# Kernel tuning notes

Measured on AMD Instinct MI355X. Metric: run time of the kernel, lower is better.

Reference implementation:

```python
import jax, jax.numpy as jnp
import numpy as np

B, C, H, W = 4, 256, 128, 128
RATION = 1
Cr = C // RATION


def conv1x1(x, Wt, b):
    # pointwise conv: [B,C,H,W] x [O,C] -> [B,O,H,W]
    return jnp.einsum('bchw,oc->bohw', x, Wt) + b[None, :, None, None]


def setup_inputs() -> dict:
    key = jax.random.key(0)
    ks = jax.random.split(key, 10)
    s_in = 1.0 / np.sqrt(C)
    s_up = 1.0 / np.sqrt(Cr)
    return {
        'x': jax.random.normal(ks[0], (B, C, H, W), dtype=jnp.float32),
        'Wq': jax.random.normal(ks[1], (Cr, C), dtype=jnp.float32) * s_in,
        'bq': jax.random.normal(ks[2], (Cr,), dtype=jnp.float32) * s_in,
        'Wk': jax.random.normal(ks[3], (Cr, C), dtype=jnp.float32) * s_in,
        'bk': jax.random.normal(ks[4], (Cr,), dtype=jnp.float32) * s_in,
        'Wv': jax.random.normal(ks[5], (Cr, C), dtype=jnp.float32) * s_in,
        'bv': jax.random.normal(ks[6], (Cr,), dtype=jnp.float32) * s_in,
        'Wu': jax.random.normal(ks[7], (C, Cr), dtype=jnp.float32) * s_up,
        'bu': jax.random.normal(ks[8], (C,), dtype=jnp.float32) * s_up,
        'gamma': jax.random.normal(ks[9], (1,), dtype=jnp.float32) * 0.1,
    }


def reference(x, Wq, bq, Wk, bk, Wv, bv, Wu, bu, gamma):
    b, c, h, w = x.shape
    # Q/K/V: relu(1x1 conv), then raw contiguous reshape [B,Cr,H,W] -> [B,W,Cr*H]
    x_Qw = jax.nn.relu(conv1x1(x, Wq, bq)).reshape(b, w, -1)              # [B, W, Cr*H]
    x_Kw = jnp.swapaxes(jax.nn.relu(conv1x1(x, Wk, bk)).reshape(b, w, -1), 1, 2)  # [B, Cr*H, W]
    x_Vw = jnp.swapaxes(jax.nn.relu(conv1x1(x, Wv, bv)).reshape(b, w, -1), 1, 2)  # [B, Cr*H, W]
    # attention over Width axis; softmax over dim=1 as in the original
    attn = jax.nn.softmax(jnp.matmul(x_Qw, x_Kw), axis=1)                 # [B, W, W]
    out1 = jnp.matmul(x_Vw, attn)                                         # [B, Cr*H, W]
    out = out1.reshape(b, c // RATION, h, w) * gamma
    out_w = conv1x1(out, Wu, bu)                                          # [B, C, H, W]
    return (out_w, x_Qw, x_Kw, x_Vw, gamma, attn)
```

## Files before the change

### kernel.cpp

```cpp
#include <hip/hip_runtime.h>
#include <hip/hip_bf16.h>


typedef __attribute__((ext_vector_type(8))) short bf16x8;
typedef __attribute__((ext_vector_type(4))) float f4;

#define MFMA16(a, b, c) __builtin_amdgcn_mfma_f32_16x16x32_bf16(a, b, c, 0, 0, 0)

__device__ __forceinline__ unsigned short f2bf(float f) {
  union { float f; unsigned u; } v; v.f = f;
  unsigned r = v.u + 0x7fffu + ((v.u >> 16) & 1u);
  return (unsigned short)(r >> 16);
}
__device__ __forceinline__ float bf2f(unsigned short h) {
  union { unsigned u; float f; } v; v.u = ((unsigned)h) << 16;
  return v.f;
}
__device__ __forceinline__ void splitf(float f, unsigned short &hi, unsigned short &lo) {
  unsigned short h = f2bf(f);
  hi = h; lo = f2bf(f - bf2f(h));
}

__device__ __forceinline__ void split8t(float4 a, float4 b, bf16x8 &hi, bf16x8 &lo) {
  union { bf16x8 v; unsigned u[4]; } uh, ul;
  const unsigned* ua = (const unsigned*)&a;
  const unsigned* ub = (const unsigned*)&b;
  const float* fa = (const float*)&a;
  const float* fb = (const float*)&b;
#pragma unroll
  for (int e = 0; e < 2; ++e) {
    uh.u[e]     = __builtin_amdgcn_perm(ua[2*e+1], ua[2*e], 0x07060302u);
    uh.u[2 + e] = __builtin_amdgcn_perm(ub[2*e+1], ub[2*e], 0x07060302u);
    union { float f; unsigned u; } p0, p1, q0, q1;
    p0.u = ua[2*e] & 0xffff0000u;   p1.u = ua[2*e+1] & 0xffff0000u;
    p0.f = fa[2*e] - p0.f;          p1.f = fa[2*e+1] - p1.f;
    ul.u[e] = __builtin_amdgcn_perm(p1.u, p0.u, 0x07060302u);
    q0.u = ub[2*e] & 0xffff0000u;   q1.u = ub[2*e+1] & 0xffff0000u;
    q0.f = fb[2*e] - q0.f;          q1.f = fb[2*e+1] - q1.f;
    ul.u[2 + e] = __builtin_amdgcn_perm(q1.u, q0.u, 0x07060302u);
  }
  hi = uh.v; lo = ul.v;
}

__device__ __forceinline__ bf16x8 pack8t(float4 a, float4 b) {
  union { bf16x8 v; unsigned u[4]; } r;
  const unsigned* ua = (const unsigned*)&a;
  const unsigned* ub = (const unsigned*)&b;
  r.u[0] = __builtin_amdgcn_perm(ua[1], ua[0], 0x07060302u);
  r.u[1] = __builtin_amdgcn_perm(ua[3], ua[2], 0x07060302u);
  r.u[2] = __builtin_amdgcn_perm(ub[1], ub[0], 0x07060302u);
  r.u[3] = __builtin_amdgcn_perm(ub[3], ub[2], 0x07060302u);
  return r.v;
}

__global__ __launch_bounds__(256) void k_prep(
    const float* __restrict__ Wq, const float* __restrict__ Wk,
    const float* __restrict__ Wv, const float* __restrict__ Wu,
    unsigned short* __restrict__ wqh, unsigned short* __restrict__ wql,
    unsigned short* __restrict__ wkh, unsigned short* __restrict__ wkl,
    unsigned short* __restrict__ wvh, unsigned short* __restrict__ wuh) {
  const int i = blockIdx.x * 256 + threadIdx.x;
  unsigned short h, lo2;
  splitf(Wq[i], h, lo2); wqh[i] = h; wql[i] = lo2;
  splitf(Wk[i], h, lo2); wkh[i] = h; wkl[i] = lo2;
  wvh[i] = f2bf(Wv[i]);
  wuh[i] = f2bf(Wu[i]);
}

__global__ __launch_bounds__(256, 4) void k_qkv(
    const float* __restrict__ x,
    const unsigned short* __restrict__ wqh, const unsigned short* __restrict__ wql,
    const unsigned short* __restrict__ wkh, const unsigned short* __restrict__ wkl,
    const unsigned short* __restrict__ wvh,
    const float* __restrict__ bq, const float* __restrict__ bk,
    const float* __restrict__ bv,
    float* __restrict__ outQ, float* __restrict__ outKT, float* __restrict__ outVT,
    float* __restrict__ K2f) {
  const int pb = blockIdx.x, b = blockIdx.y;
  const int p0 = pb * 32;
  const int t = threadIdx.x;

  __shared__ __align__(16) unsigned short xthi[32][264];
  __shared__ __align__(16) unsigned short xtlo[32][264];
  float (*tbuf)[132] = reinterpret_cast<float (*)[132]>(&xtlo[0][0]);

  {
    const int cp = t & 127;
    const int hh = (t >> 7) * 16;
    const float* r0 = x + ((size_t)b * 256 + 2 * cp) * 16384 + p0 + hh;
    const float* r1 = r0 + 16384;
#pragma unroll
    for (int q = 0; q < 4; ++q) {
      float4 v0 = *(const float4*)(r0 + 4 * q);
      float4 v1 = *(const float4*)(r1 + 4 * q);
      const unsigned* u0 = (const unsigned*)&v0;
      const unsigned* u1 = (const unsigned*)&v1;
      const float* f0 = (const float*)&v0;
      const float* f1 = (const float*)&v1;
#pragma unroll
      for (int e = 0; e < 4; ++e) {
        const int p = hh + 4 * q + e;
        *(unsigned*)&xthi[p][2 * cp] = __builtin_amdgcn_perm(u1[e], u0[e], 0x07060302u);
        union { float f; unsigned u; } l0, l1;
        l0.u = u0[e] & 0xffff0000u;  l1.u = u1[e] & 0xffff0000u;
        l0.f = f0[e] - l0.f;         l1.f = f1[e] - l1.f;
        *(unsigned*)&xtlo[p][2 * cp] = __builtin_amdgcn_perm(l1.u, l0.u, 0x07060302u);
      }
    }
  }
  __syncthreads();

  const int wv = t >> 6, l = t & 63;
  const int lr = l & 15, lkq = l >> 4, lk = lkq * 8;
  const size_t ob = (size_t)b * 4194304;
  const f4 fz = {0.f, 0.f, 0.f, 0.f};
  f4 acc[4][2];

#define CONV_PASS(WHI, WLO, SPLIT)                                        \
  {                                                                       \
    _Pragma("unroll") for (int mt = 0; mt < 4; ++mt)                      \
    _Pragma("unroll") for (int nt = 0; nt < 2; ++nt) acc[mt][nt] = fz;    \
    _Pragma("unroll 1") for (int kk = 0; kk < 8; ++kk) {                  \
      const int c0 = kk * 32 + lk;                                        \
      bf16x8 ahi[4], alo[4], bhi[2], blo[2];                              \
      _Pragma("unroll") for (int mt = 0; mt < 4; ++mt) {                  \
        const int o = wv * 64 + mt * 16 + lr;                             \
        ahi[mt] = *(const bf16x8*)(WHI + o * 256 + c0);                   \
        if (SPLIT) alo[mt] = *(const bf16x8*)(WLO + o * 256 + c0);        \
      }                                                                   \
      _Pragma("unroll") for (int nt = 0; nt < 2; ++nt) {                  \
        bhi[nt] = *(const bf16x8*)&xthi[nt * 16 + lr][c0];                \
        if (SPLIT) blo[nt] = *(const bf16x8*)&xtlo[nt * 16 + lr][c0];     \
      }                                                                   \
      _Pragma("unroll") for (int mt = 0; mt < 4; ++mt)                    \
      _Pragma("unroll") for (int nt = 0; nt < 2; ++nt) {                  \
        acc[mt][nt] = MFMA16(ahi[mt], bhi[nt], acc[mt][nt]);              \
        if (SPLIT) {                                                      \
          acc[mt][nt] = MFMA16(ahi[mt], blo[nt], acc[mt][nt]);            \
          acc[mt][nt] = MFMA16(alo[mt], bhi[nt], acc[mt][nt]);            \
        }                                                                 \
      }                                                                   \
    }                                                                     \
  }

#define TRANSPOSE_OUT(DST)                                                   \
  _Pragma("unroll") for (int par = 0; par < 2; ++par) {                      \
    __syncthreads();                                                         \
    _Pragma("unroll") for (int mt = 0; mt < 4; ++mt)                         \
    _Pragma("unroll") for (int m = 0; m < 2; ++m) {                          \
      const int i = wv * 32 + mt * 8 + lkq * 2 + m;                          \
      const int e = par + 2 * m;       \
      _Pragma("unroll") for (int nt = 0; nt < 2; ++nt)                       \
        tbuf[nt * 16 + lr][i] = acc[mt][nt][e];                              \
    }                                                                        \
    __syncthreads();                                                         \
    {                                                                        \
      const int pr = t >> 3, c4 = (t & 7) * 16;                              \
      float* dst = DST + ob + (size_t)(par * 16384 + p0 + pr) * 128 + c4;    \
      _Pragma("unroll") for (int q2 = 0; q2 < 4; ++q2)                       \
        *(float4*)(dst + 4 * q2) = *(const float4*)&tbuf[pr][c4 + 4 * q2];   \
    }                                                                        \
  }

  CONV_PASS(wqh, wql, 1)
  {
    const int rbase = wv * 64 + lkq * 4;
#pragma unroll
    for (int mt = 0; mt < 4; ++mt)
#pragma unroll
      for (int e = 0; e < 4; ++e) {
        const int o = rbase + mt * 16 + e;
        const float bb = bq[o];
#pragma unroll
        for (int nt = 0; nt < 2; ++nt)
          outQ[ob + (size_t)o * 16384 + (p0 + nt * 16 + lr)] =
              fmaxf(acc[mt][nt][e] + bb, 0.0f);
      }
  }

  CONV_PASS(wkh, wkl, 1)
  {
    const int rbase = wv * 64 + lkq * 4;
#pragma unroll
    for (int mt = 0; mt < 4; ++mt)
#pragma unroll
      for (int e = 0; e < 4; ++e) {
        const int o = rbase + mt * 16 + e;
        const float bb = bk[o];
#pragma unroll
        for (int nt = 0; nt < 2; ++nt) {
          const float v = fmaxf(acc[mt][nt][e] + bb, 0.0f);
          acc[mt][nt][e] = v;
          K2f[ob + (size_t)o * 16384 + (p0 + nt * 16 + lr)] = v;
        }
      }
  }
  TRANSPOSE_OUT(outKT)

  CONV_PASS(wvh, wvh, 0)
  {
    const int rbase = wv * 64 + lkq * 4;
#pragma unroll
    for (int mt = 0; mt < 4; ++mt)
#pragma unroll
      for (int e = 0; e < 4; ++e) {
        const int o = rbase + mt * 16 + e;
        const float bb = bv[o];
#pragma unroll
        for (int nt = 0; nt < 2; ++nt)
          acc[mt][nt][e] = fmaxf(acc[mt][nt][e] + bb, 0.0f);
      }
  }
  TRANSPOSE_OUT(outVT)
#undef CONV_PASS
#undef TRANSPOSE_OUT
}

__global__ __launch_bounds__(512, 4) void k_qk(
    const float* __restrict__ Q2, const float* __restrict__ K2f,
    float* __restrict__ Spart) {
  const int s = blockIdx.x, b = blockIdx.y;
  const int t = threadIdx.x;
  const int wvv = t >> 6, l = t & 63;
  const int wm = (wvv >> 2) * 64, wn = (wvv & 3) * 32;
  const int lr = l & 15, lkq = l >> 4, lk = lkq * 8;
  const size_t qb = (size_t)b * 4194304;
  const int jb = s * 256;
  const f4 fz = {0.f, 0.f, 0.f, 0.f};
  f4 acc[4][2];
#pragma unroll
  for (int mt = 0; mt < 4; ++mt)
#pragma unroll
    for (int nt = 0; nt < 2; ++nt) acc[mt][nt] = fz;

#pragma unroll 1
  for (int kk = 0; kk < 8; ++kk) {
    const int j = jb + kk * 32 + lk;
    bf16x8 ahi[4], alo[4], bhi[2], blo[2];
#pragma unroll
    for (int mt = 0; mt < 4; ++mt) {
      const float* r = Q2 + qb + (size_t)(wm + mt * 16 + lr) * 32768 + j;
      split8t(*(const float4*)r, *(const float4*)(r + 4), ahi[mt], alo[mt]);
    }
#pragma unroll
    for (int nt = 0; nt < 2; ++nt) {
      const float* r = K2f + qb + (size_t)(wn + nt * 16 + lr) * 32768 + j;
      split8t(*(const float4*)r, *(const float4*)(r + 4), bhi[nt], blo[nt]);
    }
#pragma unroll
    for (int mt = 0; mt < 4; ++mt)
#pragma unroll
      for (int nt = 0; nt < 2; ++nt) {
        acc[mt][nt] = MFMA16(ahi[mt], bhi[nt], acc[mt][nt]);
        acc[mt][nt] = MFMA16(ahi[mt], blo[nt], acc[mt][nt]);
        acc[mt][nt] = MFMA16(alo[mt], bhi[nt], acc[mt][nt]);
      }
  }
  float* out = Spart + ((size_t)(b * 128 + s)) * 16384;
#pragma unroll
  for (int mt = 0; mt < 4; ++mt)
#pragma unroll
    for (int e = 0; e < 4; ++e) {
      const int i1 = wm + mt * 16 + lkq * 4 + e;
#pragma unroll
      for (int nt = 0; nt < 2; ++nt)
        out[i1 * 128 + (wn + nt * 16 + lr)] = acc[mt][nt][e];
    }
}

__global__ __launch_bounds__(256) void k_sred(
    const float* __restrict__ Spart, float* __restrict__ S) {
  const int e = blockIdx.x * 256 + threadIdx.x;
  const int b = blockIdx.y;
  const float* p = Spart + (size_t)b * 128 * 16384 + e;
  float s0 = 0.f, s1 = 0.f, s2 = 0.f, s3 = 0.f;
#pragma unroll 4
  for (int s = 0; s < 128; s += 4) {
    s0 += p[(size_t)s * 16384];
    s1 += p[(size_t)(s + 1) * 16384];
    s2 += p[(size_t)(s + 2) * 16384];
    s3 += p[(size_t)(s + 3) * 16384];
  }
  S[b * 16384 + e] = (s0 + s1) + (s2 + s3);
}

__global__ __launch_bounds__(256) void k_softmax(
    const float* __restrict__ S, const float* __restrict__ gin,
    float* __restrict__ attnO, float* __restrict__ gammaO,
    unsigned short* __restrict__ attnTg) {
  const int cb = blockIdx.x, b = blockIdx.y;
  const int t = threadIdx.x;
  const int col = cb * 8 + (t >> 5);
  const int r = t & 31;
  const float* Sb = S + b * 16384;
  float v[4];
#pragma unroll
  for (int j = 0; j < 4; ++j) v[j] = Sb[(r + 32 * j) * 128 + col];
  float m = fmaxf(fmaxf(v[0], v[1]), fmaxf(v[2], v[3]));
#pragma unroll
  for (int k = 16; k >= 1; k >>= 1) m = fmaxf(m, __shfl_xor(m, k, 32));
  float sum = 0.f;
#pragma unroll
  for (int j = 0; j < 4; ++j) { v[j] = expf(v[j] - m); sum += v[j]; }
#pragma unroll
  for (int k = 16; k >= 1; k >>= 1) sum += __shfl_xor(sum, k, 32);
  const float inv = 1.0f / sum;
  const float g = gin[0];
#pragma unroll
  for (int j = 0; j < 4; ++j) {
    const float p2 = v[j] * inv;
    attnO[b * 16384 + (r + 32 * j) * 128 + col] = p2;
    attnTg[(size_t)b * 16384 + (size_t)col * 128 + (r + 32 * j)] = f2bf(p2 * g);
  }
  if (b == 0 && cb == 0 && t == 0) gammaO[0] = gin[0];
}

__global__ __launch_bounds__(256) void k_pv(
    const float* __restrict__ VT, const unsigned short* __restrict__ attnTg,
    unsigned short* __restrict__ outb) {
  const int jblk = blockIdx.x, b = blockIdx.y;
  const int t = threadIdx.x;
  const int wvv = t >> 6, l = t & 63;
  const int lr = l & 15, lkq = l >> 4, lk = lkq * 8;
  const size_t vb = (size_t)b * 4194304;
  const int j0 = jblk * 256 + wvv * 64;
  const f4 fz = {0.f, 0.f, 0.f, 0.f};
  f4 acc[4][8];
#pragma unroll
  for (int mt = 0; mt < 4; ++mt)
#pragma unroll
    for (int nt = 0; nt < 8; ++nt) acc[mt][nt] = fz;

#pragma unroll
  for (int kk = 0; kk < 4; ++kk) {
    const int k0 = kk * 32 + lk;
    bf16x8 av[4], bt[8];
#pragma unroll
    for (int mt = 0; mt < 4; ++mt) {
      const float* r = VT + vb + (size_t)(j0 + mt * 16 + lr) * 128 + k0;
      av[mt] = pack8t(*(const float4*)r, *(const float4*)(r + 4));
    }
#pragma unroll
    for (int nt = 0; nt < 8; ++nt)
      bt[nt] = *(const bf16x8*)(attnTg + (size_t)b * 16384 +
                                (size_t)(nt * 16 + lr) * 128 + k0);
#pragma unroll
    for (int mt = 0; mt < 4; ++mt)
#pragma unroll
      for (int nt = 0; nt < 8; ++nt)
        acc[mt][nt] = MFMA16(av[mt], bt[nt], acc[mt][nt]);
  }
#pragma unroll
  for (int mt = 0; mt < 4; ++mt)
#pragma unroll
    for (int e = 0; e < 4; ++e) {
      const int j = j0 + mt * 16 + lkq * 4 + e;
#pragma unroll
      for (int nt = 0; nt < 8; ++nt)
        outb[vb + (size_t)j * 128 + (nt * 16 + lr)] = f2bf(acc[mt][nt][e]);
    }
}

__global__ __launch_bounds__(256) void k_up(
    const unsigned short* __restrict__ outb, const unsigned short* __restrict__ wuh,
    const float* __restrict__ bu, float* __restrict__ outw) {
  const int pb = blockIdx.x, b = blockIdx.y;
  const int p0 = pb * 64;
  const int t = threadIdx.x;
  __shared__ unsigned short ot[64][264];
  {
    const int cp = t & 127;
    const int ph = (t >> 7) * 32;
    const unsigned short* row0 = outb + ((size_t)b * 256 + 2 * cp) * 16384 + p0 + ph;
    const unsigned* r0 = (const unsigned*)row0;
    const unsigned* r1 = (const unsigned*)(row0 + 16384);
#pragma unroll
    for (int k = 0; k < 16; ++k) {
      const unsigned a0 = r0[k], a1 = r1[k];
      const int p = ph + 2 * k;
      *(unsigned*)&ot[p][2 * cp] = (a0 & 0xffffu) | (a1 << 16);
      *(unsigned*)&ot[p + 1][2 * cp] = (a0 >> 16) | (a1 & 0xffff0000u);
    }
  }
  __syncthreads();
  const int wv = t >> 6, l = t & 63;
  const int lr = l & 15, lkq = l >> 4, lk = lkq * 8;
  const f4 fz = {0.f, 0.f, 0.f, 0.f};
  f4 acc[4][4];
#pragma unroll
  for (int mt = 0; mt < 4; ++mt)
#pragma unroll
    for (int nt = 0; nt < 4; ++nt) acc[mt][nt] = fz;

#pragma unroll 1
  for (int kk = 0; kk < 8; ++kk) {
    const int c0 = kk * 32 + lk;
    bf16x8 a[4], bt[4];
#pragma unroll
    for (int mt = 0; mt < 4; ++mt)
      a[mt] = *(const bf16x8*)(wuh + (wv * 64 + mt * 16 + lr) * 256 + c0);
#pragma unroll
    for (int nt = 0; nt < 4; ++nt)
      bt[nt] = *(const bf16x8*)&ot[nt * 16 + lr][c0];
#pragma unroll
    for (int mt = 0; mt < 4; ++mt)
#pragma unroll
      for (int nt = 0; nt < 4; ++nt)
        acc[mt][nt] = MFMA16(a[mt], bt[nt], acc[mt][nt]);
  }
  const size_t ob2 = (size_t)b * 4194304;
  const int rbase = wv * 64 + lkq * 4;
#pragma unroll
  for (int mt = 0; mt < 4; ++mt)
#pragma unroll
    for (int e = 0; e < 4; ++e) {
      const int o = rbase + mt * 16 + e;
      const float bb = bu[o];
#pragma unroll
      for (int nt = 0; nt < 4; ++nt)
        outw[ob2 + (size_t)o * 16384 + (p0 + nt * 16 + lr)] = acc[mt][nt][e] + bb;
    }
}

extern "C" void kernel_launch(void* const* d_in, const int* in_sizes, int n_in,
                              void* d_out, int out_size, void* d_ws, size_t ws_size,
                              hipStream_t stream) {
  (void)in_sizes; (void)n_in; (void)out_size; (void)ws_size;
  const float* x  = (const float*)d_in[0];
  const float* Wq = (const float*)d_in[1];
  const float* bq = (const float*)d_in[2];
  const float* Wk = (const float*)d_in[3];
  const float* bk = (const float*)d_in[4];
  const float* Wv = (const float*)d_in[5];
  const float* bv = (const float*)d_in[6];
  const float* Wu = (const float*)d_in[7];
  const float* bu = (const float*)d_in[8];
  const float* gm = (const float*)d_in[9];

  float* dout   = (float*)d_out;
  float* outw   = dout;
  float* outQ   = dout + 16777216;
  float* outKT  = dout + 33554432;
  float* outVT  = dout + 50331648;
  float* gammaO = dout + 67108864;
  float* attnO  = dout + 67108865;

  char* wsb = (char*)d_ws;
  float* K2f   = (float*)(wsb);
  float* Spart = (float*)(wsb + 67108864);
  unsigned short* outb = (unsigned short*)(wsb + 67108864);
  float* S     = (float*)(wsb + 100663296);
  unsigned short* attnTg = (unsigned short*)(wsb + 100925440);
  unsigned short* wqh = (unsigned short*)(wsb + 101056512);
  unsigned short* wql = wqh + 65536;
  unsigned short* wkh = wql + 65536;
  unsigned short* wkl = wkh + 65536;
  unsigned short* wvh = wkl + 65536;
  unsigned short* wuh = wvh + 65536;

  k_prep<<<dim3(256), dim3(256), 0, stream>>>(Wq, Wk, Wv, Wu,
                                              wqh, wql, wkh, wkl, wvh, wuh);
  k_qkv<<<dim3(512, 4), dim3(256), 0, stream>>>(x, wqh, wql, wkh, wkl, wvh,
                                                bq, bk, bv,
                                                outQ, outKT, outVT, K2f);
  k_qk<<<dim3(128, 4), dim3(512), 0, stream>>>(outQ, K2f, Spart);
  k_sred<<<dim3(64, 4), dim3(256), 0, stream>>>(Spart, S);
  k_softmax<<<dim3(16, 4), dim3(256), 0, stream>>>(S, gm, attnO, gammaO, attnTg);
  k_pv<<<dim3(128, 4), dim3(256), 0, stream>>>(outVT, attnTg, outb);
  k_up<<<dim3(256, 4), dim3(256), 0, stream>>>(outb, wuh, bu, outw);
}
```

Measured before the change: 591.5 us.

## Drop K2f scratch copy; read K from transposed output via LDS in QK

```diff
diff --git a/kernel.cpp b/kernel.cpp
--- a/kernel.cpp
+++ b/kernel.cpp
@@ -74,47 +74,50 @@
     const unsigned short* __restrict__ wvh,
     const float* __restrict__ bq, const float* __restrict__ bk,
     const float* __restrict__ bv,
-    float* __restrict__ outQ, float* __restrict__ outKT, float* __restrict__ outVT,
-    float* __restrict__ K2f) {
-  const int pb = blockIdx.x, b = blockIdx.y;
-  const int p0 = pb * 32;
+    float* __restrict__ outQ, float* __restrict__ outKT, float* __restrict__ outVT) {
+  const int pbv = blockIdx.x, b = blockIdx.y;
   const int t = threadIdx.x;
 
   __shared__ __align__(16) unsigned short xthi[32][264];
   __shared__ __align__(16) unsigned short xtlo[32][264];
   float (*tbuf)[132] = reinterpret_cast<float (*)[132]>(&xtlo[0][0]);
-
-  {
-    const int cp = t & 127;
-    const int hh = (t >> 7) * 16;
-    const float* r0 = x + ((size_t)b * 256 + 2 * cp) * 16384 + p0 + hh;
-    const float* r1 = r0 + 16384;
-#pragma unroll
-    for (int q = 0; q < 4; ++q) {
-      float4 v0 = *(const float4*)(r0 + 4 * q);
-      float4 v1 = *(const float4*)(r1 + 4 * q);
-      const unsigned* u0 = (const unsigned*)&v0;
-      const unsigned* u1 = (const unsigned*)&v1;
-      const float* f0 = (const float*)&v0;
-      const float* f1 = (const float*)&v1;
-#pragma unroll
-      for (int e = 0; e < 4; ++e) {
-        const int p = hh + 4 * q + e;
-        *(unsigned*)&xthi[p][2 * cp] = __builtin_amdgcn_perm(u1[e], u0[e], 0x07060302u);
-        union { float f; unsigned u; } l0, l1;
-        l0.u = u0[e] & 0xffff0000u;  l1.u = u1[e] & 0xffff0000u;
-        l0.f = f0[e] - l0.f;         l1.f = f1[e] - l1.f;
-        *(unsigned*)&xtlo[p][2 * cp] = __builtin_amdgcn_perm(l1.u, l0.u, 0x07060302u);
-      }
-    }
-  }
-  __syncthreads();
 
   const int wv = t >> 6, l = t & 63;
   const int lr = l & 15, lkq = l >> 4, lk = lkq * 8;
   const size_t ob = (size_t)b * 4194304;
   const f4 fz = {0.f, 0.f, 0.f, 0.f};
   f4 acc[4][2];
+
+#pragma unroll 1
+  for (int st = 0; st < 2; ++st) {
+    const int p0 = pbv * 64 + st * 32;
+    __syncthreads();
+
+    {
+      const int cp = t & 127;
+      const int hh = (t >> 7) * 16;
+      const float* r0 = x + ((size_t)b * 256 + 2 * cp) * 16384 + p0 + hh;
+      const float* r1 = r0 + 16384;
+#pragma unroll
+      for (int q = 0; q < 4; ++q) {
+        float4 v0 = *(const float4*)(r0 + 4 * q);
+        float4 v1 = *(const float4*)(r1 + 4 * q);
+        const unsigned* u0 = (const unsigned*)&v0;
+        const unsigned* u1 = (const unsigned*)&v1;
+        const float* f0 = (const float*)&v0;
+        const float* f1 = (const float*)&v1;
+#pragma unroll
+        for (int e = 0; e < 4; ++e) {
+          const int p = hh + 4 * q + e;
+          *(unsigned*)&xthi[p][2 * cp] = __builtin_amdgcn_perm(u1[e], u0[e], 0x07060302u);
+          union { float f; unsigned u; } l0, l1;
+          l0.u = u0[e] & 0xffff0000u;  l1.u = u1[e] & 0xffff0000u;
+          l0.f = f0[e] - l0.f;         l1.f = f1[e] - l1.f;
+          *(unsigned*)&xtlo[p][2 * cp] = __builtin_amdgcn_perm(l1.u, l0.u, 0x07060302u);
+        }
+      }
+    }
+    __syncthreads();
 
 #define CONV_PASS(WHI, WLO, SPLIT)                                        \
   {                                                                       \
@@ -149,7 +152,7 @@
     _Pragma("unroll") for (int mt = 0; mt < 4; ++mt)                         \
     _Pragma("unroll") for (int m = 0; m < 2; ++m) {                          \
       const int i = wv * 32 + mt * 8 + lkq * 2 + m;                          \
-      const int e = par + 2 * m;       \
+      const int e = par + 2 * m;                                             \
       _Pragma("unroll") for (int nt = 0; nt < 2; ++nt)                       \
         tbuf[nt * 16 + lr][i] = acc[mt][nt][e];                              \
     }                                                                        \
@@ -162,62 +165,60 @@
     }                                                                        \
   }
 
-  CONV_PASS(wqh, wql, 1)
-  {
-    const int rbase = wv * 64 + lkq * 4;
-#pragma unroll
-    for (int mt = 0; mt < 4; ++mt)
-#pragma unroll
-      for (int e = 0; e < 4; ++e) {
-        const int o = rbase + mt * 16 + e;
-        const float bb = bq[o];
-#pragma unroll
-        for (int nt = 0; nt < 2; ++nt)
-          outQ[ob + (size_t)o * 16384 + (p0 + nt * 16 + lr)] =
-              fmaxf(acc[mt][nt][e] + bb, 0.0f);
-      }
-  }
-
-  CONV_PASS(wkh, wkl, 1)
-  {
-    const int rbase = wv * 64 + lkq * 4;
-#pragma unroll
-    for (int mt = 0; mt < 4; ++mt)
-#pragma unroll
-      for (int e = 0; e < 4; ++e) {
-        const int o = rbase + mt * 16 + e;
-        const float bb = bk[o];
-#pragma unroll
-        for (int nt = 0; nt < 2; ++nt) {
-          const float v = fmaxf(acc[mt][nt][e] + bb, 0.0f);
-          acc[mt][nt][e] = v;
-          K2f[ob + (size_t)o * 16384 + (p0 + nt * 16 + lr)] = v;
+    CONV_PASS(wqh, wql, 1)
+    {
+      const int rbase = wv * 64 + lkq * 4;
+#pragma unroll
+      for (int mt = 0; mt < 4; ++mt)
+#pragma unroll
+        for (int e = 0; e < 4; ++e) {
+          const int o = rbase + mt * 16 + e;
+          const float bb = bq[o];
+#pragma unroll
+          for (int nt = 0; nt < 2; ++nt)
+            outQ[ob + (size_t)o * 16384 + (p0 + nt * 16 + lr)] =
+                fmaxf(acc[mt][nt][e] + bb, 0.0f);
         }
-      }
-  }
-  TRANSPOSE_OUT(outKT)
-
-  CONV_PASS(wvh, wvh, 0)
-  {
-    const int rbase = wv * 64 + lkq * 4;
-#pragma unroll
-    for (int mt = 0; mt < 4; ++mt)
-#pragma unroll
-      for (int e = 0; e < 4; ++e) {
-        const int o = rbase + mt * 16 + e;
-        const float bb = bv[o];
-#pragma unroll
-        for (int nt = 0; nt < 2; ++nt)
-          acc[mt][nt][e] = fmaxf(acc[mt][nt][e] + bb, 0.0f);
-      }
-  }
-  TRANSPOSE_OUT(outVT)
+    }
+
+    CONV_PASS(wkh, wkl, 1)
+    {
+      const int rbase = wv * 64 + lkq * 4;
+#pragma unroll
+      for (int mt = 0; mt < 4; ++mt)
+#pragma unroll
+        for (int e = 0; e < 4; ++e) {
+          const int o = rbase + mt * 16 + e;
+          const float bb = bk[o];
+#pragma unroll
+          for (int nt = 0; nt < 2; ++nt)
+            acc[mt][nt][e] = fmaxf(acc[mt][nt][e] + bb, 0.0f);
+        }
+    }
+    TRANSPOSE_OUT(outKT)
+
+    CONV_PASS(wvh, wvh, 0)
+    {
+      const int rbase = wv * 64 + lkq * 4;
+#pragma unroll
+      for (int mt = 0; mt < 4; ++mt)
+#pragma unroll
+        for (int e = 0; e < 4; ++e) {
+          const int o = rbase + mt * 16 + e;
+          const float bb = bv[o];
+#pragma unroll
+          for (int nt = 0; nt < 2; ++nt)
+            acc[mt][nt][e] = fmaxf(acc[mt][nt][e] + bb, 0.0f);
+        }
+    }
+    TRANSPOSE_OUT(outVT)
 #undef CONV_PASS
 #undef TRANSPOSE_OUT
-}
-
-__global__ __launch_bounds__(512, 4) void k_qk(
-    const float* __restrict__ Q2, const float* __restrict__ K2f,
+  }
+}
+
+__global__ __launch_bounds__(512, 2) void k_qk(
+    const float* __restrict__ Q2, const float* __restrict__ KT,
     float* __restrict__ Spart) {
   const int s = blockIdx.x, b = blockIdx.y;
   const int t = threadIdx.x;
@@ -226,6 +227,10 @@
   const int lr = l & 15, lkq = l >> 4, lk = lkq * 8;
   const size_t qb = (size_t)b * 4194304;
   const int jb = s * 256;
+
+  __shared__ __align__(16) unsigned short khi[128][136];
+  __shared__ __align__(16) unsigned short klo[128][136];
+
   const f4 fz = {0.f, 0.f, 0.f, 0.f};
   f4 acc[4][2];
 #pragma unroll
@@ -234,28 +239,51 @@
     for (int nt = 0; nt < 2; ++nt) acc[mt][nt] = fz;
 
 #pragma unroll 1
-  for (int kk = 0; kk < 8; ++kk) {
-    const int j = jb + kk * 32 + lk;
-    bf16x8 ahi[4], alo[4], bhi[2], blo[2];
-#pragma unroll
-    for (int mt = 0; mt < 4; ++mt) {
-      const float* r = Q2 + qb + (size_t)(wm + mt * 16 + lr) * 32768 + j;
-      split8t(*(const float4*)r, *(const float4*)(r + 4), ahi[mt], alo[mt]);
-    }
-#pragma unroll
-    for (int nt = 0; nt < 2; ++nt) {
-      const float* r = K2f + qb + (size_t)(wn + nt * 16 + lr) * 32768 + j;
-      split8t(*(const float4*)r, *(const float4*)(r + 4), bhi[nt], blo[nt]);
-    }
-#pragma unroll
-    for (int mt = 0; mt < 4; ++mt)
+  for (int jt = 0; jt < 2; ++jt) {
+    const int jsub = jb + jt * 128;
+    __syncthreads();
+#pragma unroll
+    for (int it = 0; it < 8; ++it) {
+      const int idx = it * 512 + t;
+      const int jg = idx >> 5, i2c = (idx & 31) * 4;
+      float4 v = *(const float4*)(KT + qb + (size_t)(jsub + jg) * 128 + i2c);
+      const float* fv = (const float*)&v;
+#pragma unroll
+      for (int e = 0; e < 4; ++e) {
+        union { float f; unsigned u; } w; w.f = fv[e];
+        const unsigned short hi = (unsigned short)(w.u >> 16);
+        union { unsigned u; float f; } hf; hf.u = (unsigned)hi << 16;
+        khi[i2c + e][jg] = hi;
+        klo[i2c + e][jg] = f2bf(w.f - hf.f);
+      }
+    }
+    __syncthreads();
+
+#pragma unroll 1
+    for (int kk = 0; kk < 4; ++kk) {
+      const int jloc = kk * 32 + lk;
+      bf16x8 ahi[4], alo[4], bhi[2], blo[2];
+#pragma unroll
+      for (int mt = 0; mt < 4; ++mt) {
+        const float* r = Q2 + qb + (size_t)(wm + mt * 16 + lr) * 32768 + jsub + jloc;
+        split8t(*(const float4*)r, *(const float4*)(r + 4), ahi[mt], alo[mt]);
+      }
 #pragma unroll
       for (int nt = 0; nt < 2; ++nt) {
-        acc[mt][nt] = MFMA16(ahi[mt], bhi[nt], acc[mt][nt]);
-        acc[mt][nt] = MFMA16(ahi[mt], blo[nt], acc[mt][nt]);
-        acc[mt][nt] = MFMA16(alo[mt], bhi[nt], acc[mt][nt]);
+        bhi[nt] = *(const bf16x8*)&khi[wn + nt * 16 + lr][jloc];
+        blo[nt] = *(const bf16x8*)&klo[wn + nt * 16 + lr][jloc];
       }
-  }
+#pragma unroll
+      for (int mt = 0; mt < 4; ++mt)
+#pragma unroll
+        for (int nt = 0; nt < 2; ++nt) {
+          acc[mt][nt] = MFMA16(ahi[mt], bhi[nt], acc[mt][nt]);
+          acc[mt][nt] = MFMA16(ahi[mt], blo[nt], acc[mt][nt]);
+          acc[mt][nt] = MFMA16(alo[mt], bhi[nt], acc[mt][nt]);
+        }
+    }
+  }
+
   float* out = Spart + ((size_t)(b * 128 + s)) * 16384;
 #pragma unroll
   for (int mt = 0; mt < 4; ++mt)
@@ -364,62 +392,70 @@
 __global__ __launch_bounds__(256) void k_up(
     const unsigned short* __restrict__ outb, const unsigned short* __restrict__ wuh,
     const float* __restrict__ bu, float* __restrict__ outw) {
-  const int pb = blockIdx.x, b = blockIdx.y;
-  const int p0 = pb * 64;
+  const int pbv = blockIdx.x, b = blockIdx.y;
   const int t = threadIdx.x;
   __shared__ unsigned short ot[64][264];
-  {
-    const int cp = t & 127;
-    const int ph = (t >> 7) * 32;
-    const unsigned short* row0 = outb + ((size_t)b * 256 + 2 * cp) * 16384 + p0 + ph;
-    const unsigned* r0 = (const unsigned*)row0;
-    const unsigned* r1 = (const unsigned*)(row0 + 16384);
-#pragma unroll
-    for (int k = 0; k < 16; ++k) {
-      const unsigned a0 = r0[k], a1 = r1[k];
-      const int p = ph + 2 * k;
-      *(unsigned*)&ot[p][2 * cp] = (a0 & 0xffffu) | (a1 << 16);
-      *(unsigned*)&ot[p + 1][2 * cp] = (a0 >> 16) | (a1 & 0xffff0000u);
-    }
-  }
-  __syncthreads();
   const int wv = t >> 6, l = t & 63;
   const int lr = l & 15, lkq = l >> 4, lk = lkq * 8;
   const f4 fz = {0.f, 0.f, 0.f, 0.f};
-  f4 acc[4][4];
-#pragma unroll
-  for (int mt = 0; mt < 4; ++mt)
-#pragma unroll
-    for (int nt = 0; nt < 4; ++nt) acc[mt][nt] = fz;
+  const size_t ob2 = (size_t)b * 4194304;
 
 #pragma unroll 1
-  for (int kk = 0; kk < 8; ++kk) {
-    const int c0 = kk * 32 + lk;
-    bf16x8 a[4], bt[4];
+  for (int st = 0; st < 2; ++st) {
+    const int p0 = pbv * 128 + st * 64;
+    __syncthreads();
+    {
+      const int cp = t & 127;
+      const int ph = (t >> 7) * 32;
+      const unsigned short* row0 = outb + ((size_t)b * 256 + 2 * cp) * 16384 + p0 + ph;
+      const unsigned* r0 = (const unsigned*)row0;
+      const unsigned* r1 = (const unsigned*)(row0 + 16384);
+#pragma unroll
+      for (int k = 0; k < 16; ++k) {
+        const unsigned a0 = r0[k], a1 = r1[k];
+        const int p = ph + 2 * k;
+        *(unsigned*)&ot[p][2 * cp] = (a0 & 0xffffu) | (a1 << 16);
+        *(unsigned*)&ot[p + 1][2 * cp] = (a0 >> 16) | (a1 & 0xffff0000u);
+      }
+    }
+    __syncthreads();
+
+    f4 acc[4][4];
 #pragma unroll
     for (int mt = 0; mt < 4; ++mt)
-      a[mt] = *(const bf16x8*)(wuh + (wv * 64 + mt * 16 + lr) * 256 + c0);
-#pragma unroll
-    for (int nt = 0; nt < 4; ++nt)
-      bt[nt] = *(const bf16x8*)&ot[nt * 16 + lr][c0];
+#pragma unroll
+      for (int nt = 0; nt < 4; ++nt) acc[mt][nt] = fz;
+
+#pragma unroll 1
+    for (int kk = 0; kk < 8; ++kk) {
+      const int c0 = kk * 32 + lk;
+      bf16x8 a[4], bt[4];
+#pragma unroll
+      for (int mt = 0; mt < 4; ++mt)
+        a[mt] = *(const bf16x8*)(wuh + (wv * 64 + mt * 16 + lr) * 256 + c0);
+#pragma unroll
+      for (int nt = 0; nt < 4; ++nt)
+        bt[nt] = *(const bf16x8*)&ot[nt * 16 + lr][c0];
+#pragma unroll
+      for (int mt = 0; mt < 4; ++mt)
+#pragma unroll
+        for (int nt = 0; nt < 4; ++nt)
+          acc[mt][nt] = MFMA16(a[mt], bt[nt], acc[mt][nt]);
+    }
+    const int rbase = wv * 64 + lkq * 4;
 #pragma unroll
     for (int mt = 0; mt < 4; ++mt)
 #pragma unroll
-      for (int nt = 0; nt < 4; ++nt)
-        acc[mt][nt] = MFMA16(a[mt], bt[nt], acc[mt][nt]);
-  }
-  const size_t ob2 = (size_t)b * 4194304;
-  const int rbase = wv * 64 + lkq * 4;
-#pragma unroll
-  for (int mt = 0; mt < 4; ++mt)
-#pragma unroll
-    for (int e = 0; e < 4; ++e) {
-      const int o = rbase + mt * 16 + e;
-      const float bb = bu[o];
-#pragma unroll
-      for (int nt = 0; nt < 4; ++nt)
-        outw[ob2 + (size_t)o * 16384 + (p0 + nt * 16 + lr)] = acc[mt][nt][e] + bb;
-    }
+      for (int e = 0; e < 4; ++e) {
+        const int o = rbase + mt * 16 + e;
+        const float bb = bu[o];
+#pragma unroll
+        for (int nt = 0; nt < 4; ++nt)
+          __builtin_nontemporal_store(
+              acc[mt][nt][e] + bb,
+              &outw[ob2 + (size_t)o * 16384 + (p0 + nt * 16 + lr)]);
+      }
+  }
 }
 
 extern "C" void kernel_launch(void* const* d_in, const int* in_sizes, int n_in,
@@ -446,12 +482,11 @@
   float* attnO  = dout + 67108865;
 
   char* wsb = (char*)d_ws;
-  float* K2f   = (float*)(wsb);
-  float* Spart = (float*)(wsb + 67108864);
-  unsigned short* outb = (unsigned short*)(wsb + 67108864);
-  float* S     = (float*)(wsb + 100663296);
-  unsigned short* attnTg = (unsigned short*)(wsb + 100925440);
-  unsigned short* wqh = (unsigned short*)(wsb + 101056512);
+  float* Spart = (float*)(wsb);
+  unsigned short* outb = (unsigned short*)(wsb);
+  float* S     = (float*)(wsb + 33554432);
+  unsigned short* attnTg = (unsigned short*)(wsb + 33816576);
+  unsigned short* wqh = (unsigned short*)(wsb + 33947648);
   unsigned short* wql = wqh + 65536;
   unsigned short* wkh = wql + 65536;
   unsigned short* wkl = wkh + 65536;
@@ -460,12 +495,12 @@
 
   k_prep<<<dim3(256), dim3(256), 0, stream>>>(Wq, Wk, Wv, Wu,
                                               wqh, wql, wkh, wkl, wvh, wuh);
-  k_qkv<<<dim3(512, 4), dim3(256), 0, stream>>>(x, wqh, wql, wkh, wkl, wvh,
+  k_qkv<<<dim3(256, 4), dim3(256), 0, stream>>>(x, wqh, wql, wkh, wkl, wvh,
                                                 bq, bk, bv,
-                                                outQ, outKT, outVT, K2f);
-  k_qk<<<dim3(128, 4), dim3(512), 0, stream>>>(outQ, K2f, Spart);
+                                                outQ, outKT, outVT);
+  k_qk<<<dim3(128, 4), dim3(512), 0, stream>>>(outQ, outKT, Spart);
   k_sred<<<dim3(64, 4), dim3(256), 0, stream>>>(Spart, S);
   k_softmax<<<dim3(16, 4), dim3(256), 0, stream>>>(S, gm, attnO, gammaO, attnTg);
   k_pv<<<dim3(128, 4), dim3(256), 0, stream>>>(outVT, attnTg, outb);
-  k_up<<<dim3(256, 4), dim3(256), 0, stream>>>(outb, wuh, bu, outw);
-}
+  k_up<<<dim3(128, 4), dim3(256), 0, stream>>>(outb, wuh, bu, outw);
+}
```

After: 623.5 us. 1.05x slower.
